# Kernel optimization log

Hardware: AMD Instinct MI355X
Metric: run time of the kernel (lower is better)

The kernel has to match this reference:

```python
import jax, jax.numpy as jnp
import numpy as np

N_LOC, N_EVT, E = 100000, 200000, 1000000
F_LOC, F_EVT, H = 128, 128, 64


def setup_inputs() -> dict:
    key = jax.random.key(0)
    ks = jax.random.split(key, 12)
    s = lambda k, shp: jax.random.normal(k, shp, dtype=jnp.float32) * (1.0 / np.sqrt(shp[0]))
    return {
        "loc_x": jax.random.normal(ks[0], (N_LOC, F_LOC), dtype=jnp.float32),
        "evt_x": jax.random.normal(ks[1], (N_EVT, F_EVT), dtype=jnp.float32),
        "edge_index": jax.random.randint(ks[2], (2, E), 0, N_LOC, dtype=jnp.int64),
        # projections (stored as (in, out))
        "W_loc": s(ks[3], (F_LOC, H)), "b_loc": jnp.zeros((H,), jnp.float32),
        "W_evt": s(ks[4], (F_EVT, H)), "b_evt": jnp.zeros((H,), jnp.float32),
        # SAGEConv: lin_l (on aggregated src, with bias), lin_r (on dst root, no bias)
        "W_l": s(ks[5], (H, H)), "b_l": jnp.zeros((H,), jnp.float32),
        "W_r": s(ks[6], (H, H)),
        # head MLP
        "W_h1": s(ks[7], (H, H // 2)), "b_h1": jnp.zeros((H // 2,), jnp.float32),
        "W_h2": s(ks[8], (H // 2, 1)), "b_h2": jnp.zeros((1,), jnp.float32),
    }


def reference(loc_x, evt_x, edge_index, W_loc, b_loc, W_evt, b_evt,
              W_l, b_l, W_r, W_h1, b_h1, W_h2, b_h2):
    # node projections + ReLU
    loc_h = jax.nn.relu(loc_x @ W_loc + b_loc)   # [N_loc, H]
    evt_h = jax.nn.relu(evt_x @ W_evt + b_evt)   # [N_evt, H]

    src, dst = edge_index[0], edge_index[1]      # event -> location
    n_loc = loc_h.shape[0]
    # mean aggregation of source (event) features onto destination (location) nodes
    msg_sum = jax.ops.segment_sum(evt_h[src], dst, num_segments=n_loc)   # [N_loc, H]
    cnt = jax.ops.segment_sum(jnp.ones_like(dst, dtype=loc_h.dtype), dst,
                              num_segments=n_loc)
    agg = msg_sum / jnp.maximum(cnt, 1.0)[:, None]
    # SAGEConv: lin_l(agg) + lin_r(root), then ReLU
    loc_h = jax.nn.relu(agg @ W_l + b_l + loc_h @ W_r)

    # prediction head
    h = jax.nn.relu(loc_h @ W_h1 + b_h1)
    logits = (h @ W_h2 + b_h2)[:, 0]             # [N_loc]
    return logits
```

## Files before the change

kernel.cpp:

```cpp
#include <hip/hip_runtime.h>


#define N_LOC 100000
#define N_EVT 200000
#define E_CNT 1000000
#define NTILES 6250
#define NBKT   256
#define BKT_L  391
#define CAPG   6000
#define QCAP   32
#define BKT_BLK 512
#define PERB   1954

#define PROJ_EVT_BLK 1536
#define PROJ_LOC_BLK 768
#define PROJ_BLK_TOT (PROJ_EVT_BLK + PROJ_LOC_BLK)
#define PB_TOT (PROJ_BLK_TOT + BKT_BLK)
#define EVT_TILES 12500
#define LOC_TILES 6250
#define HEAD_BLK  1024

typedef __attribute__((ext_vector_type(8))) short short8;
typedef __attribute__((ext_vector_type(4))) float floatx4;
typedef __attribute__((ext_vector_type(8))) unsigned short ushort8v;

__device__ __forceinline__ float b2f(unsigned short u) {
    unsigned int x = ((unsigned int)u) << 16;
    return __builtin_bit_cast(float, x);
}
__device__ __forceinline__ unsigned short f2b(float f) {
    unsigned int x = __builtin_bit_cast(unsigned int, f);
    unsigned int r = (x + 0x7fffu + ((x >> 16) & 1u)) >> 16;
    return (unsigned short)r;
}
__device__ __forceinline__ float loadf(const void* p, int f32, size_t i) {
    return f32 ? ((const float*)p)[i] : b2f(((const unsigned short*)p)[i]);
}

__global__ __launch_bounds__(256) void prep_kernel(
    const void* t0, const void* t1, const int* eidx,
    const void* t3, const void* t4, const void* t5, const void* t6,
    const void* t7, const void* t8, const void* t9, const void* t10,
    const void* t11, const void* t12, const void* t13,
    int* flags, int* gbc, unsigned short* __restrict__ wp_all) {
    int b = blockIdx.x, tid = threadIdx.x;
    __shared__ int s0, s1;

    if (b == 14) { gbc[tid] = 0; return; }

    if (b >= 15) {
        int pb = b - 15;
        const void* W; int K, N, bstart, off;
        if (pb < 4)       { W = t5;  K = 128; N = 64; bstart = 0;  off = 0; }
        else if (pb < 8)  { W = t3;  K = 128; N = 64; bstart = 4;  off = 8192; }
        else if (pb < 10) { W = t7;  K = 64;  N = 64; bstart = 8;  off = 16384; }
        else if (pb < 12) { W = t9;  K = 64;  N = 64; bstart = 10; off = 20480; }
        else              { W = t10; K = 64;  N = 32; bstart = 12; off = 24576; }
        if (tid == 0) s0 = 0;
        __syncthreads();
        int nsamp = 2 * K * N; if (nsamp > 1024) nsamp = 1024;
        const unsigned short* h = (const unsigned short*)W;
        int susp = 0;
        for (int i = tid; i < nsamp; i += 256)
            if (((h[i] >> 7) & 0xFF) >= 0x90) susp++;
        if (susp) atomicAdd(&s0, susp);
        __syncthreads();
        int f32 = (s0 * 16 >= nsamp) ? 1 : 0;

        int idx  = (pb - bstart) * 256 + tid;
        int nk   = K >> 5;
        int f    = idx >> 6;
        int lane = idx & 63;
        int t  = f / nk;
        int kk = f - t * nk;
        int n  = t * 16 + (lane & 15);
        int k0 = kk * 32 + (lane >> 4) * 8;
        unsigned short tmp[8];
#pragma unroll
        for (int j = 0; j < 8; ++j) {
            size_t src = (size_t)(k0 + j) * N + n;
            tmp[j] = f32 ? f2b(((const float*)W)[src])
                         : ((const unsigned short*)W)[src];
        }
#pragma unroll
        for (int j = 0; j < 8; ++j) wp_all[(size_t)off + (size_t)idx * 8 + j] = tmp[j];
        return;
    }

    if (tid == 0) { s0 = 0; s1 = 0; }
    __syncthreads();
    if (b == 13) {
        if (tid < 128) {
            if (eidx[2 * tid] != 0) atomicAdd(&s0, 1);
            if (eidx[2 * tid + 1] != 0) atomicAdd(&s1, 1);
        }
        __syncthreads();
        if (tid == 0) flags[2] = (s1 == 0 && s0 > 32) ? 1 : 0;
        return;
    }
    const void* ptrs[13] = {t0, t1, t3, t4, t5, t6, t7, t8, t9, t10, t11, t12, t13};
    const int   cnts[13] = {12800000, 25600000, 8192, 64, 8192, 64,
                            4096, 64, 4096, 2048, 32, 32, 1};
    const int   slot[13] = {0, 1, 3, 4, 5, 6, 7, 8, 9, 10, 11, 12, 13};
    int nsamp = 2 * cnts[b];
    if (nsamp > 1024) nsamp = 1024;
    const unsigned short* h = (const unsigned short*)ptrs[b];
    int susp = 0;
    for (int i = tid; i < nsamp; i += 256)
        if (((h[i] >> 7) & 0xFF) >= 0x90) susp++;
    if (susp) atomicAdd(&s0, susp);
    __syncthreads();
    if (tid == 0) flags[slot[b]] = (s0 * 16 >= nsamp) ? 1 : 0;
}

__global__ __launch_bounds__(256) void proj_bucket_kernel(
    const void* __restrict__ evt_x, const void* __restrict__ loc_x,
    const unsigned short* __restrict__ wp_all,
    const void* __restrict__ b_evt, const void* __restrict__ b_loc,
    unsigned short* __restrict__ evt_h, unsigned short* __restrict__ loc_h,
    const int* __restrict__ eidx, uint2* __restrict__ bkt,
    int* __restrict__ gbc, const int* __restrict__ flags) {
    __shared__ uint2 queue[NBKT][QCAP];
    __shared__ int qcnt[NBKT];
    int b = blockIdx.x;
    int g = b / 11, r = b % 11;
    int tid = threadIdx.x;

    if (r >= 9) {
        int blk = g * 2 + (r - 9);
        qcnt[tid] = 0;
        __syncthreads();
        int f64 = flags[2];
        const long long* e64 = (const long long*)eidx;
        int e0 = blk * PERB;
        int e1 = e0 + PERB; if (e1 > E_CNT) e1 = E_CNT;
        const int rounds = (PERB + 255) / 256;

        for (int rr = 0; rr < rounds; ++rr) {
            int e = e0 + rr * 256 + tid;
            if (e < e1) {
                int src, dst;
                if (f64) { src = (int)e64[e]; dst = (int)e64[E_CNT + e]; }
                else     { src = eidx[e];     dst = eidx[E_CNT + e]; }
                if ((unsigned)dst < (unsigned)N_LOC && (unsigned)src < (unsigned)N_EVT) {
                    int bk = dst / BKT_L;
                    int pos = atomicAdd(&qcnt[bk], 1);
                    if (pos < QCAP) {
                        queue[bk][pos] = make_uint2((unsigned)src, (unsigned)dst);
                    } else {
                        int p = atomicAdd(&gbc[bk], 1);
                        if (p < CAPG) bkt[(size_t)bk * CAPG + p] = make_uint2(src, dst);
                    }
                }
            }
            __syncthreads();
            int n = qcnt[tid]; if (n > QCAP) n = QCAP;
            while (n >= 16) {
                int gp = atomicAdd(&gbc[tid], 16);
                if (gp + 16 <= CAPG) {
                    uint2* d = bkt + (size_t)tid * CAPG + gp;
#pragma unroll
                    for (int j = 0; j < 16; ++j) d[j] = queue[tid][j];
                }
#pragma unroll
                for (int j = 16; j < QCAP; ++j) queue[tid][j - 16] = queue[tid][j];
                n -= 16;
            }
            qcnt[tid] = n;
            __syncthreads();
        }
        int n = qcnt[tid]; if (n > QCAP) n = QCAP;
        if (n > 0) {
            int gp = atomicAdd(&gbc[tid], n);
            for (int j = 0; j < n; ++j)
                if (gp + j < CAPG) bkt[(size_t)tid * CAPG + gp + j] = queue[tid][j];
        }
        return;
    }

    unsigned short* bs = (unsigned short*)&queue[0][0];
    int blk = g * 9 + r;
    int lane = tid & 63, wv = tid >> 6;
    int l15 = lane & 15, quad = lane >> 4;

    const void* X; const unsigned short* Wp; const void* bias;
    unsigned short* Y; int fx, fb, w0, nw, ntile;
    if (blk < PROJ_EVT_BLK) {
        X = evt_x; Wp = wp_all;        bias = b_evt; Y = evt_h;
        fx = flags[1]; fb = flags[6];
        w0 = blk * 4 + wv; nw = PROJ_EVT_BLK * 4; ntile = EVT_TILES;
    } else {
        X = loc_x; Wp = wp_all + 8192; bias = b_loc; Y = loc_h;
        fx = flags[0]; fb = flags[4];
        w0 = (blk - PROJ_EVT_BLK) * 4 + wv; nw = PROJ_LOC_BLK * 4; ntile = LOC_TILES;
    }

    {
        const short8* src = reinterpret_cast<const short8*>(Wp);
        short8* dst = reinterpret_cast<short8*>(bs);
#pragma unroll
        for (int i = 0; i < 4; ++i) dst[tid + i * 256] = src[tid + i * 256];
    }
    __syncthreads();

    float bv[4];
#pragma unroll
    for (int q = 0; q < 4; ++q) bv[q] = loadf(bias, fb, q * 16 + l15);

    if (w0 >= ntile) return;

    auto mfma_store = [&](const short8* a, int t) {
        floatx4 acc[4];
#pragma unroll
        for (int q = 0; q < 4; ++q) acc[q] = (floatx4)0.0f;
#pragma unroll
        for (int q = 0; q < 4; ++q) {
            short8 bq[4];
#pragma unroll
            for (int kk = 0; kk < 4; ++kk)
                bq[kk] = *reinterpret_cast<const short8*>(
                    &bs[((q * 4 + kk) * 64 + lane) * 8]);
#pragma unroll
            for (int kk = 0; kk < 4; ++kk)
                acc[q] = __builtin_amdgcn_mfma_f32_16x16x32_bf16(
                    a[kk], bq[kk], acc[q], 0, 0, 0);
        }
#pragma unroll
        for (int q = 0; q < 4; ++q)
#pragma unroll
            for (int rr = 0; rr < 4; ++rr) {
                float v = acc[q][rr] + bv[q];
                v = v > 0.0f ? v : 0.0f;
                Y[(size_t)(t * 16 + quad * 4 + rr) * 64 + q * 16 + l15] = f2b(v);
            }
    };

    if (fx) {
        const float* Xf = (const float*)X;
        float4 pf[8];
        auto issueF = [&](int t) {
            const float* xr = Xf + (size_t)(t * 16 + l15) * 128 + quad * 8;
#pragma unroll
            for (int kk = 0; kk < 4; ++kk) {
                pf[kk * 2]     = *reinterpret_cast<const float4*>(xr + kk * 32);
                pf[kk * 2 + 1] = *reinterpret_cast<const float4*>(xr + kk * 32 + 4);
            }
        };
        issueF(w0);
        for (int t = w0; t < ntile; t += nw) {
            short8 a[4];
#pragma unroll
            for (int kk = 0; kk < 4; ++kk) {
                float4 p0 = pf[kk * 2], p1 = pf[kk * 2 + 1];
                short8 v;
                v[0] = (short)f2b(p0.x); v[1] = (short)f2b(p0.y);
                v[2] = (short)f2b(p0.z); v[3] = (short)f2b(p0.w);
                v[4] = (short)f2b(p1.x); v[5] = (short)f2b(p1.y);
                v[6] = (short)f2b(p1.z); v[7] = (short)f2b(p1.w);
                a[kk] = v;
            }
            int tn = t + nw;
            if (tn < ntile) issueF(tn);
            mfma_store(a, t);
        }
    } else {
        const unsigned short* Xh = (const unsigned short*)X;
        short8 an[4];
        auto issueH = [&](int t) {
            const unsigned short* xr = Xh + (size_t)(t * 16 + l15) * 128 + quad * 8;
#pragma unroll
            for (int kk = 0; kk < 4; ++kk)
                an[kk] = *reinterpret_cast<const short8*>(xr + kk * 32);
        };
        issueH(w0);
        for (int t = w0; t < ntile; t += nw) {
            short8 a[4];
#pragma unroll
            for (int kk = 0; kk < 4; ++kk) a[kk] = an[kk];
            int tn = t + nw;
            if (tn < ntile) issueH(tn);
            mfma_store(a, t);
        }
    }
}

__global__ __launch_bounds__(512) void csr_build_kernel(
    const uint2* __restrict__ bkt, const int* __restrict__ gbc,
    int* __restrict__ rowptr, int* __restrict__ csr) {
    __shared__ int sg[256];
    __shared__ int lcnt[512];
    __shared__ int lscan[512];
    __shared__ int lcsr[CAPG];
    int b = blockIdx.x, tid = threadIdx.x;
    int loc0 = b * BKT_L;
    int nloc = N_LOC - loc0; if (nloc > BKT_L) nloc = BKT_L;

    if (tid < 256) {
        int gv = gbc[tid]; if (gv > CAPG) gv = CAPG;
        sg[tid] = gv;
    }
    __syncthreads();
    for (int d = 1; d < 256; d <<= 1) {
        int x = (tid < 256 && tid >= d) ? sg[tid - d] : 0;
        __syncthreads();
        if (tid < 256) sg[tid] += x;
        __syncthreads();
    }
    int cntE = gbc[b]; if (cntE > CAPG) cntE = CAPG;
    int base = sg[b] - cntE;
    const uint2* bp = bkt + (size_t)b * CAPG;

    lcnt[tid] = 0;
    __syncthreads();
    for (int i = tid; i < cntE; i += 512) {
        int d = (int)bp[i].y - loc0;
        atomicAdd(&lcnt[d], 1);
    }
    __syncthreads();
    lscan[tid] = lcnt[tid];
    __syncthreads();
    for (int d = 1; d < 512; d <<= 1) {
        int v = (tid >= d) ? lscan[tid - d] : 0;
        __syncthreads();
        lscan[tid] += v;
        __syncthreads();
    }
    for (int i = tid; i < nloc; i += 512) {
        int excl = lscan[i] - lcnt[i];
        rowptr[loc0 + i] = base + excl;
        lcnt[i] = excl;
    }
    if (b == NBKT - 1 && tid == 0) rowptr[N_LOC] = base + cntE;
    __syncthreads();
    for (int i = tid; i < cntE; i += 512) {
        uint2 pr = bp[i];
        int d = (int)pr.y - loc0;
        int p = atomicAdd(&lcnt[d], 1);
        if (p < CAPG) lcsr[p] = (int)pr.x;
    }
    __syncthreads();
    for (int i = tid; i < cntE; i += 512) csr[base + i] = lcsr[i];
}

__global__ __launch_bounds__(256) void aggregate_kernel(
    const unsigned short* __restrict__ evt_h,
    const int* __restrict__ rowptr, const int* __restrict__ csr,
    unsigned short* __restrict__ agg, int N) {
    int wid  = (blockIdx.x * 256 + threadIdx.x) >> 6;
    int lane = threadIdx.x & 63;
    int eo = lane >> 3, cg = lane & 7;
    if (wid >= N) return;
    int e0 = rowptr[wid], e1 = rowptr[wid + 1];
    float a[8];
#pragma unroll
    for (int k = 0; k < 8; ++k) a[k] = 0.0f;

    int j = e0;
    for (; j + 16 <= e1; j += 16) {
        int s0 = csr[j + eo];
        int s1 = csr[j + 8 + eo];
        ushort8v v0 = *reinterpret_cast<const ushort8v*>(
            evt_h + (size_t)s0 * 64 + cg * 8);
        ushort8v v1 = *reinterpret_cast<const ushort8v*>(
            evt_h + (size_t)s1 * 64 + cg * 8);
#pragma unroll
        for (int k = 0; k < 8; ++k) a[k] += b2f(v0[k]) + b2f(v1[k]);
    }
    for (; j < e1; j += 8) {
        int jj = j + eo;
        bool c = jj < e1;
        int s = csr[c ? jj : j];
        ushort8v v = *reinterpret_cast<const ushort8v*>(
            evt_h + (size_t)s * 64 + cg * 8);
        if (c) {
#pragma unroll
            for (int k = 0; k < 8; ++k) a[k] += b2f(v[k]);
        }
    }
#pragma unroll
    for (int k = 0; k < 8; ++k) {
        a[k] += __shfl_xor(a[k], 8);
        a[k] += __shfl_xor(a[k], 16);
        a[k] += __shfl_xor(a[k], 32);
    }
    float inv = (e1 > e0) ? 1.0f / (float)(e1 - e0) : 0.0f;
    if (eo == 0) {
        ushort8v o;
#pragma unroll
        for (int k = 0; k < 8; ++k) o[k] = f2b(a[k] * inv);
        *reinterpret_cast<ushort8v*>(agg + (size_t)wid * 64 + cg * 8) = o;
    }
}

__global__ __launch_bounds__(256, 3) void head_kernel(
    const unsigned short* __restrict__ agg,
    const unsigned short* __restrict__ loc_h,
    const unsigned short* __restrict__ wp_all,
    const void* __restrict__ bl, const void* __restrict__ bh1,
    const void* __restrict__ wh2, const void* __restrict__ bh2,
    void* __restrict__ out, const int* __restrict__ flags) {
    __shared__ unsigned short bls[4096];
    __shared__ unsigned short brs[4096];
    __shared__ unsigned short b1s[2048];
    __shared__ unsigned short h2s[4][16 * 64];
    int tid = threadIdx.x, lane = tid & 63, wv = tid >> 6;
    int l15 = lane & 15, quad = lane >> 4;
    int fbl = flags[8], fbh1 = flags[11], fwh2 = flags[12], fbh2 = flags[13];
    int fout = flags[0];
    const unsigned short* wp_l  = wp_all + 16384;
    const unsigned short* wp_r  = wp_all + 20480;
    const unsigned short* wp_h1 = wp_all + 24576;

    {
        const short8* sl = reinterpret_cast<const short8*>(wp_l);
        const short8* sr = reinterpret_cast<const short8*>(wp_r);
        const short8* s1 = reinterpret_cast<const short8*>(wp_h1);
        short8* dl = reinterpret_cast<short8*>(bls);
        short8* dr = reinterpret_cast<short8*>(brs);
        short8* d1 = reinterpret_cast<short8*>(b1s);
        dl[tid] = sl[tid]; dl[tid + 256] = sl[tid + 256];
        dr[tid] = sr[tid]; dr[tid + 256] = sr[tid + 256];
        d1[tid] = s1[tid];
    }
    __syncthreads();

    float bbl[4], bh1v[2], w2v[2];
#pragma unroll
    for (int q = 0; q < 4; ++q) bbl[q] = loadf(bl, fbl, q * 16 + l15);
#pragma unroll
    for (int q = 0; q < 2; ++q) {
        bh1v[q] = loadf(bh1, fbh1, q * 16 + l15);
        w2v[q]  = loadf(wh2, fwh2, q * 16 + l15);
    }
    float bb2 = loadf(bh2, fbh2, 0);

    const int NW = HEAD_BLK * 4;
    int w0 = blockIdx.x * 4 + wv;
    if (w0 >= NTILES) return;

    short8 c0[4], c1[4];

    auto issue = [&](short8* c, int t) {
        int m = t * 16 + l15;
#pragma unroll
        for (int kk = 0; kk < 2; ++kk) {
            c[kk]     = *reinterpret_cast<const short8*>(
                agg + (size_t)m * 64 + kk * 32 + quad * 8);
            c[2 + kk] = *reinterpret_cast<const short8*>(
                loc_h + (size_t)m * 64 + kk * 32 + quad * 8);
        }
    };

    auto compute = [&](const short8* c, int tile) {
        floatx4 acc[4];
#pragma unroll
        for (int q = 0; q < 4; ++q) acc[q] = (floatx4)0.0f;
#pragma unroll
        for (int q = 0; q < 4; ++q) {
            short8 bwl[2], bwr[2];
#pragma unroll
            for (int kk = 0; kk < 2; ++kk) {
                bwl[kk] = *reinterpret_cast<const short8*>(
                    &bls[((q * 2 + kk) * 64 + lane) * 8]);
                bwr[kk] = *reinterpret_cast<const short8*>(
                    &brs[((q * 2 + kk) * 64 + lane) * 8]);
            }
#pragma unroll
            for (int kk = 0; kk < 2; ++kk) {
                acc[q] = __builtin_amdgcn_mfma_f32_16x16x32_bf16(
                    c[kk], bwl[kk], acc[q], 0, 0, 0);
                acc[q] = __builtin_amdgcn_mfma_f32_16x16x32_bf16(
                    c[2 + kk], bwr[kk], acc[q], 0, 0, 0);
            }
        }
#pragma unroll
        for (int q = 0; q < 4; ++q)
#pragma unroll
            for (int rr = 0; rr < 4; ++rr) {
                float v = acc[q][rr] + bbl[q];
                v = v > 0.0f ? v : 0.0f;
                h2s[wv][(quad * 4 + rr) * 64 + q * 16 + l15] = f2b(v);
            }
        short8 aH[2];
#pragma unroll
        for (int kk = 0; kk < 2; ++kk)
            aH[kk] = *reinterpret_cast<const short8*>(
                &h2s[wv][l15 * 64 + kk * 32 + quad * 8]);

        floatx4 a1[2];
#pragma unroll
        for (int q = 0; q < 2; ++q) a1[q] = (floatx4)0.0f;
#pragma unroll
        for (int q = 0; q < 2; ++q) {
            short8 bw1[2];
#pragma unroll
            for (int kk = 0; kk < 2; ++kk)
                bw1[kk] = *reinterpret_cast<const short8*>(
                    &b1s[((q * 2 + kk) * 64 + lane) * 8]);
#pragma unroll
            for (int kk = 0; kk < 2; ++kk)
                a1[q] = __builtin_amdgcn_mfma_f32_16x16x32_bf16(
                    aH[kk], bw1[kk], a1[q], 0, 0, 0);
        }

        float s[4] = {0.f, 0.f, 0.f, 0.f};
#pragma unroll
        for (int q = 0; q < 2; ++q)
#pragma unroll
            for (int rr = 0; rr < 4; ++rr) {
                float v = a1[q][rr] + bh1v[q];
                v = v > 0.0f ? v : 0.0f;
                s[rr] += v * w2v[q];
            }
#pragma unroll
        for (int rr = 0; rr < 4; ++rr) {
            s[rr] += __shfl_xor(s[rr], 1);
            s[rr] += __shfl_xor(s[rr], 2);
            s[rr] += __shfl_xor(s[rr], 4);
            s[rr] += __shfl_xor(s[rr], 8);
        }
#pragma unroll
        for (int rr = 0; rr < 4; ++rr) {
            if (l15 == rr) {
                int row = tile * 16 + quad * 4 + rr;
                float v = s[rr] + bb2;
                if (fout) ((float*)out)[row] = v;
                else      ((unsigned short*)out)[row] = f2b(v);
            }
        }
    };

    issue(c0, w0);
    int t = w0;
    while (true) {
        int tn = t + NW;
        bool hn = tn < NTILES;
        if (hn) issue(c1, tn);
        compute(c0, t);
        if (!hn) break;
        t = tn; tn = t + NW; hn = tn < NTILES;
        if (hn) issue(c0, tn);
        compute(c1, t);
        if (!hn) break;
        t = tn;
    }
}

extern "C" void kernel_launch(void* const* d_in, const int* in_sizes, int n_in,
                              void* d_out, int out_size, void* d_ws, size_t ws_size,
                              hipStream_t stream) {
    (void)in_sizes; (void)n_in; (void)out_size; (void)ws_size;
    const void* loc_x = d_in[0];
    const void* evt_x = d_in[1];
    const int*  eidx  = (const int*)d_in[2];
    const void* W_loc = d_in[3];
    const void* b_loc = d_in[4];
    const void* W_evt = d_in[5];
    const void* b_evt = d_in[6];
    const void* W_l   = d_in[7];
    const void* b_l   = d_in[8];
    const void* W_r   = d_in[9];
    const void* W_h1  = d_in[10];
    const void* b_h1  = d_in[11];
    const void* W_h2  = d_in[12];
    const void* b_h2  = d_in[13];

    char* ws = (char*)d_ws;
    unsigned short* evt_h  = (unsigned short*)(ws);
    unsigned short* loc_h  = (unsigned short*)(ws + 25600000);
    int*            csr    = (int*)(ws + 38400000);
    int*            rowptr = (int*)(ws + 42400000);
    int*            gbc    = (int*)(ws + 42800016);
    unsigned short* wp_all = (unsigned short*)(ws + 42802064);
    int*            flags  = (int*)(ws + 42855312);
    uint2*          bkt    = (uint2*)(ws + 42855376);
    unsigned short* agg    = (unsigned short*)(ws + 42855376);

    prep_kernel<<<28, 256, 0, stream>>>(
        loc_x, evt_x, eidx, W_loc, b_loc, W_evt, b_evt,
        W_l, b_l, W_r, W_h1, b_h1, W_h2, b_h2,
        flags, gbc, wp_all);

    proj_bucket_kernel<<<PB_TOT, 256, 0, stream>>>(
        evt_x, loc_x, wp_all, b_evt, b_loc, evt_h, loc_h,
        eidx, bkt, gbc, flags);

    csr_build_kernel<<<NBKT, 512, 0, stream>>>(bkt, gbc, rowptr, csr);

    aggregate_kernel<<<(N_LOC + 3) / 4, 256, 0, stream>>>(evt_h, rowptr, csr,
                                                          agg, N_LOC);

    head_kernel<<<HEAD_BLK, 256, 0, stream>>>(
        agg, loc_h, wp_all, b_l, b_h1, W_h2, b_h2, d_out, flags);
}
```

Baseline: 288.0 us.

## Fuse CSR build into projection/bucket kernel using global completion counter spin-wait

Moves the CSR construction into extra trailing blocks of the projection/bucketing kernel. The bucket blocks increment a global counter when they finish, and the CSR blocks spin-wait on that counter, so one kernel launch is removed and CSR building can overlap with the tail of the projection work. This relies on forward progress: the spinning blocks are scheduled last and must not starve the bucket blocks of residency. The CSR blocks also shrink from 512 to 256 threads, and shared memory is unified into a single buffer.

```diff
diff --git a/kernel.cpp b/kernel.cpp
--- a/kernel.cpp
+++ b/kernel.cpp
@@ -16,6 +16,7 @@
 #define PROJ_LOC_BLK 768
 #define PROJ_BLK_TOT (PROJ_EVT_BLK + PROJ_LOC_BLK)
 #define PB_TOT (PROJ_BLK_TOT + BKT_BLK)
+#define PBC_TOT (PB_TOT + NBKT)
 #define EVT_TILES 12500
 #define LOC_TILES 6250
 #define HEAD_BLK  1024
@@ -46,7 +47,11 @@
     int b = blockIdx.x, tid = threadIdx.x;
     __shared__ int s0, s1;
 
-    if (b == 14) { gbc[tid] = 0; return; }
+    if (b == 14) {
+        gbc[tid] = 0;
+        if (tid == 0) gbc[256] = 0;
+        return;
+    }
 
     if (b >= 15) {
         int pb = b - 15;
@@ -113,20 +118,87 @@
     if (tid == 0) flags[slot[b]] = (s0 * 16 >= nsamp) ? 1 : 0;
 }
 
-__global__ __launch_bounds__(256) void proj_bucket_kernel(
+__global__ __launch_bounds__(256) void proj_bucket_csr_kernel(
     const void* __restrict__ evt_x, const void* __restrict__ loc_x,
     const unsigned short* __restrict__ wp_all,
     const void* __restrict__ b_evt, const void* __restrict__ b_loc,
     unsigned short* __restrict__ evt_h, unsigned short* __restrict__ loc_h,
     const int* __restrict__ eidx, uint2* __restrict__ bkt,
-    int* __restrict__ gbc, const int* __restrict__ flags) {
-    __shared__ uint2 queue[NBKT][QCAP];
-    __shared__ int qcnt[NBKT];
+    int* __restrict__ gbc, int* __restrict__ rowptr, int* __restrict__ csr,
+    const int* __restrict__ flags) {
+    __shared__ __align__(16) char smem[66560];
     int b = blockIdx.x;
+    int tid = threadIdx.x;
+
+    if (b >= PB_TOT) {
+        int* sg    = (int*)smem;
+        int* lcnt  = (int*)(smem + 1024);
+        int* lscan = (int*)(smem + 3072);
+        int* lcsr  = (int*)(smem + 5120);
+        int bb = b - PB_TOT;
+        if (tid == 0) {
+            while (atomicAdd(&gbc[256], 0) < BKT_BLK)
+                __builtin_amdgcn_s_sleep(32);
+        }
+        __syncthreads();
+        __threadfence();
+
+        int loc0 = bb * BKT_L;
+        int nloc = N_LOC - loc0; if (nloc > BKT_L) nloc = BKT_L;
+
+        int gv = gbc[tid]; if (gv > CAPG) gv = CAPG;
+        sg[tid] = gv;
+        __syncthreads();
+        for (int d = 1; d < 256; d <<= 1) {
+            int x = (tid >= d) ? sg[tid - d] : 0;
+            __syncthreads();
+            sg[tid] += x;
+            __syncthreads();
+        }
+        int cntE = gbc[bb]; if (cntE > CAPG) cntE = CAPG;
+        int base = sg[bb] - cntE;
+        const uint2* bp = bkt + (size_t)bb * CAPG;
+
+        int i0 = tid, i1 = tid + 256;
+        lcnt[i0] = 0; lcnt[i1] = 0;
+        __syncthreads();
+        for (int i = tid; i < cntE; i += 256) {
+            int d = (int)bp[i].y - loc0;
+            atomicAdd(&lcnt[d], 1);
+        }
+        __syncthreads();
+        lscan[i0] = lcnt[i0]; lscan[i1] = lcnt[i1];
+        __syncthreads();
+        for (int d = 1; d < 512; d <<= 1) {
+            int v0 = (i0 >= d) ? lscan[i0 - d] : 0;
+            int v1 = (i1 >= d) ? lscan[i1 - d] : 0;
+            __syncthreads();
+            lscan[i0] += v0; lscan[i1] += v1;
+            __syncthreads();
+        }
+        for (int i = tid; i < nloc; i += 256) {
+            int excl = lscan[i] - lcnt[i];
+            rowptr[loc0 + i] = base + excl;
+            lcnt[i] = excl;
+        }
+        if (bb == NBKT - 1 && tid == 0) rowptr[N_LOC] = base + cntE;
+        __syncthreads();
+        for (int i = tid; i < cntE; i += 256) {
+            uint2 pr = bp[i];
+            int d = (int)pr.y - loc0;
+            int p = atomicAdd(&lcnt[d], 1);
+            if (p < CAPG) lcsr[p] = (int)pr.x;
+        }
+        __syncthreads();
+        for (int i = tid; i < cntE; i += 256) csr[base + i] = lcsr[i];
+        return;
+    }
+
     int g = b / 11, r = b % 11;
-    int tid = threadIdx.x;
 
     if (r >= 9) {
+        uint2 (*queue)[QCAP] = (uint2(*)[QCAP])smem;
+        int* qcnt = (int*)(smem + 65536);
         int blk = g * 2 + (r - 9);
         qcnt[tid] = 0;
         __syncthreads();
@@ -175,10 +247,13 @@
             for (int j = 0; j < n; ++j)
                 if (gp + j < CAPG) bkt[(size_t)tid * CAPG + gp + j] = queue[tid][j];
         }
+        __threadfence();
+        __syncthreads();
+        if (tid == 0) atomicAdd(&gbc[256], 1);
         return;
     }
 
-    unsigned short* bs = (unsigned short*)&queue[0][0];
+    unsigned short* bs = (unsigned short*)smem;
     int blk = g * 9 + r;
     int lane = tid & 63, wv = tid >> 6;
     int l15 = lane & 15, quad = lane >> 4;
@@ -282,64 +357,6 @@
             mfma_store(a, t);
         }
     }
-}
-
-__global__ __launch_bounds__(512) void csr_build_kernel(
-    const uint2* __restrict__ bkt, const int* __restrict__ gbc,
-    int* __restrict__ rowptr, int* __restrict__ csr) {
-    __shared__ int sg[256];
-    __shared__ int lcnt[512];
-    __shared__ int lscan[512];
-    __shared__ int lcsr[CAPG];
-    int b = blockIdx.x, tid = threadIdx.x;
-    int loc0 = b * BKT_L;
-    int nloc = N_LOC - loc0; if (nloc > BKT_L) nloc = BKT_L;
-
-    if (tid < 256) {
-        int gv = gbc[tid]; if (gv > CAPG) gv = CAPG;
-        sg[tid] = gv;
-    }
-    __syncthreads();
-    for (int d = 1; d < 256; d <<= 1) {
-        int x = (tid < 256 && tid >= d) ? sg[tid - d] : 0;
-        __syncthreads();
-        if (tid < 256) sg[tid] += x;
-        __syncthreads();
-    }
-    int cntE = gbc[b]; if (cntE > CAPG) cntE = CAPG;
-    int base = sg[b] - cntE;
-    const uint2* bp = bkt + (size_t)b * CAPG;
-
-    lcnt[tid] = 0;
-    __syncthreads();
-    for (int i = tid; i < cntE; i += 512) {
-        int d = (int)bp[i].y - loc0;
-        atomicAdd(&lcnt[d], 1);
-    }
-    __syncthreads();
-    lscan[tid] = lcnt[tid];
-    __syncthreads();
-    for (int d = 1; d < 512; d <<= 1) {
-        int v = (tid >= d) ? lscan[tid - d] : 0;
-        __syncthreads();
-        lscan[tid] += v;
-        __syncthreads();
-    }
-    for (int i = tid; i < nloc; i += 512) {
-        int excl = lscan[i] - lcnt[i];
-        rowptr[loc0 + i] = base + excl;
-        lcnt[i] = excl;
-    }
-    if (b == NBKT - 1 && tid == 0) rowptr[N_LOC] = base + cntE;
-    __syncthreads();
-    for (int i = tid; i < cntE; i += 512) {
-        uint2 pr = bp[i];
-        int d = (int)pr.y - loc0;
-        int p = atomicAdd(&lcnt[d], 1);
-        if (p < CAPG) lcsr[p] = (int)pr.x;
-    }
-    __syncthreads();
-    for (int i = tid; i < cntE; i += 512) csr[base + i] = lcsr[i];
 }
 
 __global__ __launch_bounds__(256) void aggregate_kernel(
@@ -581,11 +598,9 @@
         W_l, b_l, W_r, W_h1, b_h1, W_h2, b_h2,
         flags, gbc, wp_all);
 
-    proj_bucket_kernel<<<PB_TOT, 256, 0, stream>>>(
+    proj_bucket_csr_kernel<<<PBC_TOT, 256, 0, stream>>>(
         evt_x, loc_x, wp_all, b_evt, b_loc, evt_h, loc_h,
-        eidx, bkt, gbc, flags);
-
-    csr_build_kernel<<<NBKT, 512, 0, stream>>>(bkt, gbc, rowptr, csr);
+        eidx, bkt, gbc, rowptr, csr, flags);
 
     aggregate_kernel<<<(N_LOC + 3) / 4, 256, 0, stream>>>(evt_h, rowptr, csr,
                                                           agg, N_LOC);
```

After: 455.7 us. 58.2% more time.
